# Performance work log

Hardware: AMD Instinct MI355X
Metric: run time of the kernel (lower is better)

The kernel has to match this reference:

```python
import jax, jax.numpy as jnp
import numpy as np

POOL = 7
H, W, C = 200, 200, 512
NUM_ROIS = 128


def setup_inputs() -> dict:
    key = jax.random.key(0)
    k1, k2, k3 = jax.random.split(key, 3)
    img = jax.random.normal(k1, (1, H, W, C), dtype=jnp.float32)
    # (x, y, w, h) in feature-map pixels; w,h >= POOL+1 so every bin is >=1px,
    # and x+w <= W, y+h <= H so crops stay in bounds (as the original assumes).
    wh = jax.random.uniform(k2, (1, NUM_ROIS, 2), minval=float(POOL + 1), maxval=64.0)
    xy = jax.random.uniform(k3, (1, NUM_ROIS, 2)) * (jnp.array([W, H], jnp.float32) - wh)
    rois = jnp.concatenate([xy, wh], axis=-1).astype(jnp.float32)
    return {"img": img, "rois": rois, "pool_size": POOL}


def _roi_pool(x, rois, P):
    # x: (H, W, C) feature map; rois: (R, 4) as (x, y, w, h) floats.
    h_dim, w_dim, _ = x.shape
    ks = jnp.arange(P + 1, dtype=jnp.float32)
    rows = jnp.arange(h_dim)
    cols = jnp.arange(w_dim)

    def pool_one(roi):
        rx, ry, rw, rh = roi[0], roi[1], roi[2], roi[3]
        # Bin boundaries: original computes x1 = int(x + ix*w/P), x2 = int(x + (ix+1)*w/P),
        # i.e. contiguous non-overlapping segments [b[k], b[k+1]).
        bx = (rx + ks * (rw / P)).astype(jnp.int32)
        by = (ry + ks * (rh / P)).astype(jnp.int32)
        # Map each row/col to its bin id; out-of-roi pixels -> dummy segment P.
        rid = jnp.searchsorted(by, rows, side='right') - 1
        rid = jnp.where((rid < 0) | (rid >= P), P, rid)
        cid = jnp.searchsorted(bx, cols, side='right') - 1
        cid = jnp.where((cid < 0) | (cid >= P), P, cid)
        # Max-reduce rows into y-bins, then cols into x-bins (separable rect max).
        rm = jax.ops.segment_max(x, rid, num_segments=P + 1)                     # (P+1, W, C) [jy, w, c]
        cm = jax.ops.segment_max(rm.transpose(1, 0, 2), cid, num_segments=P + 1)  # (P+1, P+1, C) [ix, jy, c]
        return cm[:P, :P].transpose(1, 0, 2)  # (jy, ix, c)

    return jax.vmap(pool_one)(rois)  # (R, P, P, C)


def reference(img, rois, pool_size):
    # Output: (1, num_rois, pool_size, pool_size, channels), tf dim ordering.
    out = _roi_pool(img[0], rois[0], pool_size)
    return out[None]
```

## Files before the change

### kernel.cpp

```cpp
#include <hip/hip_runtime.h>


#define IMG_H 200
#define IMG_W 200
#define IMG_C 512
#define C4 (IMG_C / 4)
#define POOL 7
#define NROI 128

__device__ __forceinline__ float4 max4(float4 a, float4 b) {
    return make_float4(fmaxf(a.x, b.x), fmaxf(a.y, b.y),
                       fmaxf(a.z, b.z), fmaxf(a.w, b.w));
}

__global__ __launch_bounds__(128) void roi_pool_kernel(
    const float* __restrict__ img,
    const float* __restrict__ rois,
    float* __restrict__ out)
{
    const int bin = blockIdx.x % (POOL * POOL);
    const int roi = blockIdx.x / (POOL * POOL);
    const int jy = bin / POOL;
    const int ix = bin % POOL;

    const float rx = rois[roi * 4 + 0];
    const float ry = rois[roi * 4 + 1];
    const float rw = rois[roi * 4 + 2];
    const float rh = rois[roi * 4 + 3];

    const float sx = __fdiv_rn(rw, 7.0f);
    const float sy = __fdiv_rn(rh, 7.0f);
    const int x1 = (int)__fadd_rn(rx, __fmul_rn((float)ix,       sx));
    const int x2 = (int)__fadd_rn(rx, __fmul_rn((float)(ix + 1), sx));
    const int y1 = (int)__fadd_rn(ry, __fmul_rn((float)jy,       sy));
    const int y2 = (int)__fadd_rn(ry, __fmul_rn((float)(jy + 1), sy));

    const int c4 = threadIdx.x;
    const float4* __restrict__ img4 = (const float4*)img;

    float4 m0 = make_float4(-INFINITY, -INFINITY, -INFINITY, -INFINITY);
    float4 m1 = m0;

    int y = y1;
    for (; y + 2 <= y2; y += 2) {
        const float4* __restrict__ rowA = img4 + ((size_t)y       * IMG_W) * C4 + c4;
        const float4* __restrict__ rowB = img4 + ((size_t)(y + 1) * IMG_W) * C4 + c4;
        #pragma unroll 4
        for (int x = x1; x < x2; ++x) {
            float4 a = rowA[(size_t)x * C4];
            float4 b = rowB[(size_t)x * C4];
            m0 = max4(m0, a);
            m1 = max4(m1, b);
        }
    }
    if (y < y2) {
        const float4* __restrict__ rowA = img4 + ((size_t)y * IMG_W) * C4 + c4;
        #pragma unroll 4
        for (int x = x1; x < x2; ++x) {
            float4 a = rowA[(size_t)x * C4];
            m0 = max4(m0, a);
        }
    }
    float4 m = max4(m0, m1);

    float4* __restrict__ out4 = (float4*)out;
    out4[((size_t)(roi * POOL + jy) * POOL + ix) * C4 + c4] = m;
}

extern "C" void kernel_launch(void* const* d_in, const int* in_sizes, int n_in,
                              void* d_out, int out_size, void* d_ws, size_t ws_size,
                              hipStream_t stream) {
    (void)in_sizes; (void)n_in; (void)d_ws; (void)ws_size; (void)out_size;
    const float* img  = (const float*)d_in[0];
    const float* rois = (const float*)d_in[1];
    float* out = (float*)d_out;

    dim3 grid(NROI * POOL * POOL);
    dim3 block(128);
    roi_pool_kernel<<<grid, block, 0, stream>>>(img, rois, out);
}
```

Measured before the change: 142.8 us.

## Split each bin's pixels across four thread planes with shared-memory max reduction

Each block now has 512 threads arranged as four planes of 128 channel-vector threads. The planes stride over the bin's flattened pixel area and combine their partial maxima through shared memory before one plane writes the result. This spreads the serial per-bin pixel loop over more waves to raise memory-level parallelism and cut per-thread latency chains, at the cost of a barrier, shared-memory traffic and idle planes on small bins. The output store also becomes a nontemporal store.

```diff
diff --git a/kernel.cpp b/kernel.cpp
--- a/kernel.cpp
+++ b/kernel.cpp
@@ -7,13 +7,16 @@
 #define C4 (IMG_C / 4)
 #define POOL 7
 #define NROI 128
+#define PLANES 4
+
+typedef float f4v __attribute__((ext_vector_type(4)));
 
 __device__ __forceinline__ float4 max4(float4 a, float4 b) {
     return make_float4(fmaxf(a.x, b.x), fmaxf(a.y, b.y),
                        fmaxf(a.z, b.z), fmaxf(a.w, b.w));
 }
 
-__global__ __launch_bounds__(128) void roi_pool_kernel(
+__global__ __launch_bounds__(PLANES * 128, 8) void roi_pool_kernel(
     const float* __restrict__ img,
     const float* __restrict__ rois,
     float* __restrict__ out)
@@ -35,36 +38,40 @@
     const int y1 = (int)__fadd_rn(ry, __fmul_rn((float)jy,       sy));
     const int y2 = (int)__fadd_rn(ry, __fmul_rn((float)(jy + 1), sy));
 
-    const int c4 = threadIdx.x;
+    const int c4 = threadIdx.x & 127;
+    const int p  = threadIdx.x >> 7;
     const float4* __restrict__ img4 = (const float4*)img;
 
-    float4 m0 = make_float4(-INFINITY, -INFINITY, -INFINITY, -INFINITY);
-    float4 m1 = m0;
+    const int bw = x2 - x1;
+    const int bh = y2 - y1;
+    const int area = bw * bh;
 
-    int y = y1;
-    for (; y + 2 <= y2; y += 2) {
-        const float4* __restrict__ rowA = img4 + ((size_t)y       * IMG_W) * C4 + c4;
-        const float4* __restrict__ rowB = img4 + ((size_t)(y + 1) * IMG_W) * C4 + c4;
-        #pragma unroll 4
-        for (int x = x1; x < x2; ++x) {
-            float4 a = rowA[(size_t)x * C4];
-            float4 b = rowB[(size_t)x * C4];
-            m0 = max4(m0, a);
-            m1 = max4(m1, b);
-        }
+    const float4 NEG = make_float4(-INFINITY, -INFINITY, -INFINITY, -INFINITY);
+    float4 m = NEG;
+
+    int dx = p, dy = 0;
+    while (dx >= bw) { dx -= bw; ++dy; }
+    #pragma unroll 2
+    for (int i = p; i < area; i += PLANES) {
+        const size_t px = (size_t)(y1 + dy) * IMG_W + (size_t)(x1 + dx);
+        m = max4(m, img4[px * C4 + c4]);
+        dx += PLANES;
+        while (dx >= bw) { dx -= bw; ++dy; }
     }
-    if (y < y2) {
-        const float4* __restrict__ rowA = img4 + ((size_t)y * IMG_W) * C4 + c4;
-        #pragma unroll 4
-        for (int x = x1; x < x2; ++x) {
-            float4 a = rowA[(size_t)x * C4];
-            m0 = max4(m0, a);
-        }
+
+    __shared__ float4 red[PLANES - 1][C4];
+    if (p > 0) red[p - 1][c4] = m;
+    __syncthreads();
+    if (p == 0) {
+        m = max4(m, red[0][c4]);
+        m = max4(m, red[1][c4]);
+        m = max4(m, red[2][c4]);
+
+        float4* __restrict__ out4 = (float4*)out;
+        f4v* __restrict__ dst =
+            (f4v*)&out4[((size_t)(roi * POOL + jy) * POOL + ix) * C4 + c4];
+        __builtin_nontemporal_store(*(const f4v*)&m, dst);
     }
-    float4 m = max4(m0, m1);
-
-    float4* __restrict__ out4 = (float4*)out;
-    out4[((size_t)(roi * POOL + jy) * POOL + ix) * C4 + c4] = m;
 }
 
 extern "C" void kernel_launch(void* const* d_in, const int* in_sizes, int n_in,
@@ -76,6 +83,6 @@
     float* out = (float*)d_out;
 
     dim3 grid(NROI * POOL * POOL);
-    dim3 block(128);
+    dim3 block(PLANES * 128);
     roi_pool_kernel<<<grid, block, 0, stream>>>(img, rois, out);
 }
```

After: 140.2 us. No clear change (-1.8%).
